# Optimization experiments

Hardware: AMD Instinct MI355X
Metric: run time of the kernel (lower is better)

## Reference

```python
import jax, jax.numpy as jnp
import numpy as np

T, H = 4096, 2048  # seq_len, hidden/feature size (hidden == features per module code)

def setup_inputs() -> dict:
    key = jax.random.key(0)
    k1, k2, k3 = jax.random.split(key, 3)
    s = 1.0 / np.sqrt(H).astype(np.float32)
    return {
        "x": jax.random.normal(k1, (T, H), jnp.float32),
        "c0": jnp.zeros((H,), jnp.float32),
        "h0": jnp.zeros((H,), jnp.float32),
        "Wi": jax.random.normal(k2, (H, 4 * H), jnp.float32) * s,  # input kernel, gates [i,f,g,o]
        "Wh": jax.random.normal(k3, (H, 4 * H), jnp.float32) * s,  # recurrent kernel
        "b": jnp.zeros((4 * H,), jnp.float32),
    }

def reference(x, c0, h0, Wi, Wh, b):
    # Faithful to flax.linen.OptimizedLSTMCell scanned over time (gate order i,f,g,o).
    def step(carry, xt):
        c, h = carry
        y = xt @ Wi + h @ Wh + b          # (4H,)
        i, f, g, o = jnp.split(y, 4)
        i = jax.nn.sigmoid(i)
        f = jax.nn.sigmoid(f)
        g = jnp.tanh(g)
        o = jax.nn.sigmoid(o)
        c_new = f * c + i * g
        h_new = o * jnp.tanh(c_new)
        return (c_new, h_new), h_new

    (c_f, h_f), ys = jax.lax.scan(step, (c0, h0), x)
    return c_f, h_f, ys
```

## Files before the change

### kernel.cpp

```cpp
#include <hip/hip_runtime.h>
#include <math.h>

#define T_STEPS 4096
#define HDIM    2048
#define KDIM    2048
#define NG      8192
#define NREC    2048
#define NSLOT   3

typedef unsigned long long ull;

__global__ void init_ws5(const float* __restrict__ h0,
                         uint2* __restrict__ recs) {
    int d = blockIdx.x * blockDim.x + threadIdx.x;
    if (d < NSLOT * NREC) {
        int slot = d >> 11;
        int r = d & (NREC - 1);
        uint2 v;
        if (slot == 2) {
            v.x = __float_as_uint(h0[r]);
            v.y = 0u;
        } else {
            v.x = 0u;
            v.y = 0xFFFFFFFFu;
        }
        recs[d] = v;
    }
}

__global__ __launch_bounds__(256) void gemm_xwi(
    const float* __restrict__ X, const float* __restrict__ Wi,
    const float* __restrict__ bias, float* __restrict__ Y)
{
    __shared__ float As[16][65];
    __shared__ __align__(16) float Bs[16][64];
    const int tid = threadIdx.x;
    const int m0 = blockIdx.y * 64;
    const int n0 = blockIdx.x * 64;
    const int tx4 = (tid & 15) * 4;
    const int ty4 = (tid >> 4) * 4;
    const int am = tid >> 2, ak = (tid & 3) * 4;
    const int bk = tid >> 4, bn = (tid & 15) * 4;

    float acc[4][4];
#pragma unroll
    for (int i = 0; i < 4; ++i)
#pragma unroll
        for (int j = 0; j < 4; ++j) acc[i][j] = 0.f;

    for (int kt = 0; kt < KDIM; kt += 16) {
        float4 av = *reinterpret_cast<const float4*>(&X[(size_t)(m0 + am) * KDIM + kt + ak]);
        float4 bv = *reinterpret_cast<const float4*>(&Wi[(size_t)(kt + bk) * NG + n0 + bn]);
        __syncthreads();
        As[ak + 0][am] = av.x; As[ak + 1][am] = av.y;
        As[ak + 2][am] = av.z; As[ak + 3][am] = av.w;
        *reinterpret_cast<float4*>(&Bs[bk][bn]) = bv;
        __syncthreads();
#pragma unroll
        for (int k = 0; k < 16; ++k) {
            float a0 = As[k][ty4 + 0], a1 = As[k][ty4 + 1];
            float a2 = As[k][ty4 + 2], a3 = As[k][ty4 + 3];
            float4 b4 = *reinterpret_cast<const float4*>(&Bs[k][tx4]);
            acc[0][0] = fmaf(a0, b4.x, acc[0][0]); acc[0][1] = fmaf(a0, b4.y, acc[0][1]);
            acc[0][2] = fmaf(a0, b4.z, acc[0][2]); acc[0][3] = fmaf(a0, b4.w, acc[0][3]);
            acc[1][0] = fmaf(a1, b4.x, acc[1][0]); acc[1][1] = fmaf(a1, b4.y, acc[1][1]);
            acc[1][2] = fmaf(a1, b4.z, acc[1][2]); acc[1][3] = fmaf(a1, b4.w, acc[1][3]);
            acc[2][0] = fmaf(a2, b4.x, acc[2][0]); acc[2][1] = fmaf(a2, b4.y, acc[2][1]);
            acc[2][2] = fmaf(a2, b4.z, acc[2][2]); acc[2][3] = fmaf(a2, b4.w, acc[2][3]);
            acc[3][0] = fmaf(a3, b4.x, acc[3][0]); acc[3][1] = fmaf(a3, b4.y, acc[3][1]);
            acc[3][2] = fmaf(a3, b4.z, acc[3][2]); acc[3][3] = fmaf(a3, b4.w, acc[3][3]);
        }
    }
    float4 bb = *reinterpret_cast<const float4*>(&bias[n0 + tx4]);
#pragma unroll
    for (int i = 0; i < 4; ++i) {
        float4 o;
        o.x = acc[i][0] + bb.x; o.y = acc[i][1] + bb.y;
        o.z = acc[i][2] + bb.z; o.w = acc[i][3] + bb.w;
        *reinterpret_cast<float4*>(&Y[(size_t)(m0 + ty4 + i) * NG + n0 + tx4]) = o;
    }
}

__device__ __forceinline__ float fsigm(float x) { return 1.f / (1.f + __expf(-x)); }
__device__ __forceinline__ float ftanh(float x) {
    float ax = fabsf(x);
    float e  = __expf(2.f * ax);
    float t  = (e - 1.f) / (e + 1.f);
    t = (ax > 15.f) ? 1.f : t;
    return copysignf(t, x);
}

__global__ __launch_bounds__(512)
__attribute__((amdgpu_waves_per_eu(2, 2)))
void lstm_persistent(
    const float* __restrict__ Y,
    const float* __restrict__ c0,
    const float* __restrict__ Wh,
    uint2* __restrict__ recs,
    float* __restrict__ out)
{
    const int b    = blockIdx.x;
    const int tid  = threadIdx.x;
    const int lane = tid & 63;
    const int w    = tid >> 6;
    const int gg   = w >> 1;
    const int hg   = w & 1;
    const int nbase = (gg << 11) + (b << 3) + (hg << 2);

    __shared__ __align__(16) float hlds[HDIM];
    __shared__ float gates[32];
    __shared__ float c_s[8];
    __shared__ float hlast[8];

    float4 wreg[32];
#pragma unroll
    for (int j = 0; j < 8; ++j)
#pragma unroll
        for (int m = 0; m < 4; ++m) {
            const size_t k = (size_t)(4 * lane + 256 * j + m);
            wreg[j * 4 + m] = *reinterpret_cast<const float4*>(&Wh[k * NG + nbase]);
        }
#pragma unroll
    for (int i = 0; i < 32; ++i) {
        asm volatile("" : "+v"(wreg[i].x), "+v"(wreg[i].y),
                          "+v"(wreg[i].z), "+v"(wreg[i].w));
    }

    if (tid < 8) c_s[tid] = c0[b * 8 + tid];
    __syncthreads();

    int rs = 2;
    int ws = 0;

    for (int t = 0; t < T_STEPS; ++t) {
        float yv = 0.f;
        if (lane < 4) yv = Y[(size_t)t * NG + nbase + lane];

        {
            const uint2* rb = recs + (size_t)rs * NREC;
            const uint2* p0 = rb + 2 * tid;
            const uint2* p1 = rb + 1024 + 2 * tid;
            const unsigned expt = (unsigned)t;
            uint4 ra, rc;
            for (;;) {
                asm volatile("global_load_dwordx4 %0, %2, off sc0 sc1\n\t"
                             "global_load_dwordx4 %1, %3, off sc0 sc1\n\t"
                             "s_waitcnt vmcnt(0)"
                             : "=&v"(ra), "=&v"(rc)
                             : "v"(p0), "v"(p1) : "memory");
                if (__all((ra.y == expt) & (ra.w == expt) &
                          (rc.y == expt) & (rc.w == expt))) break;
                __builtin_amdgcn_s_sleep(1);
            }
            float2 d0; d0.x = __uint_as_float(ra.x); d0.y = __uint_as_float(ra.z);
            float2 d1; d1.x = __uint_as_float(rc.x); d1.y = __uint_as_float(rc.z);
            *reinterpret_cast<float2*>(&hlds[2 * tid])        = d0;
            *reinterpret_cast<float2*>(&hlds[1024 + 2 * tid]) = d1;
        }
        __syncthreads();

        float4 acc; acc.x = acc.y = acc.z = acc.w = 0.f;
#pragma unroll
        for (int j = 0; j < 8; ++j) {
            float4 h4 = reinterpret_cast<const float4*>(hlds)[lane + 64 * j];
            float4 w0 = wreg[4 * j + 0], w1 = wreg[4 * j + 1];
            float4 w2 = wreg[4 * j + 2], w3 = wreg[4 * j + 3];
            acc.x = fmaf(h4.x, w0.x, acc.x); acc.x = fmaf(h4.y, w1.x, acc.x);
            acc.x = fmaf(h4.z, w2.x, acc.x); acc.x = fmaf(h4.w, w3.x, acc.x);
            acc.y = fmaf(h4.x, w0.y, acc.y); acc.y = fmaf(h4.y, w1.y, acc.y);
            acc.y = fmaf(h4.z, w2.y, acc.y); acc.y = fmaf(h4.w, w3.y, acc.y);
            acc.z = fmaf(h4.x, w0.z, acc.z); acc.z = fmaf(h4.y, w1.z, acc.z);
            acc.z = fmaf(h4.z, w2.z, acc.z); acc.z = fmaf(h4.w, w3.z, acc.z);
            acc.w = fmaf(h4.x, w0.w, acc.w); acc.w = fmaf(h4.y, w1.w, acc.w);
            acc.w = fmaf(h4.z, w2.w, acc.w); acc.w = fmaf(h4.w, w3.w, acc.w);
        }
#pragma unroll
        for (int off = 32; off >= 1; off >>= 1) {
            acc.x += __shfl_xor(acc.x, off);
            acc.y += __shfl_xor(acc.y, off);
            acc.z += __shfl_xor(acc.z, off);
            acc.w += __shfl_xor(acc.w, off);
        }
        if (lane < 4) {
            float v = (lane == 0) ? acc.x : (lane == 1) ? acc.y
                    : (lane == 2) ? acc.z : acc.w;
            gates[gg * 8 + hg * 4 + lane] = v + yv;
        }
        __syncthreads();

        if (tid < 8) {
            float iv = gates[0 * 8 + tid];
            float fv = gates[1 * 8 + tid];
            float gv = gates[2 * 8 + tid];
            float ov = gates[3 * 8 + tid];
            float cn = fsigm(fv) * c_s[tid] + fsigm(iv) * ftanh(gv);
            float hn = fsigm(ov) * ftanh(cn);
            c_s[tid] = cn;
            hlast[tid] = hn;
            ull rec = ((ull)(unsigned)(t + 1) << 32) | (ull)__float_as_uint(hn);
            uint2* dst = recs + (size_t)ws * NREC + b * 8 + tid;
            asm volatile("global_store_dwordx2 %0, %1, off sc0 sc1"
                         :: "v"(dst), "v"(rec) : "memory");
            __builtin_nontemporal_store(hn, &out[2 * HDIM + (size_t)t * HDIM + b * 8 + tid]);
        }

        rs = ws;
        ws = (ws == 2) ? 0 : ws + 1;
    }

    if (tid < 8) {
        out[b * 8 + tid]        = c_s[tid];
        out[HDIM + b * 8 + tid] = hlast[tid];
    }
}

extern "C" void kernel_launch(void* const* d_in, const int* in_sizes, int n_in,
                              void* d_out, int out_size, void* d_ws, size_t ws_size,
                              hipStream_t stream) {
    const float* x   = (const float*)d_in[0];
    const float* c0  = (const float*)d_in[1];
    const float* h0  = (const float*)d_in[2];
    const float* Wi  = (const float*)d_in[3];
    const float* Wh  = (const float*)d_in[4];
    const float* bia = (const float*)d_in[5];
    float* out = (float*)d_out;

    char* base = (char*)d_ws;
    float* Y = (float*)base;
    base += (size_t)T_STEPS * NG * sizeof(float);
    uint2* recs = (uint2*)base;

    const int initN = NSLOT * NREC;
    hipLaunchKernelGGL(init_ws5, dim3((initN + 511) / 512), dim3(512), 0, stream,
                       h0, recs);
    hipLaunchKernelGGL(gemm_xwi, dim3(NG / 64, T_STEPS / 64), dim3(256), 0, stream,
                       x, Wi, bia, Y);

    void* args[] = { (void*)&Y, (void*)&c0, (void*)&Wh,
                     (void*)&recs, (void*)&out };
    (void)hipLaunchCooperativeKernel((const void*)lstm_persistent, dim3(256), dim3(512),
                                     args, 0, stream);
}
```

Baseline: 13.92 ms.

## Enlarge GEMM tiles to 128x128 and give each LSTM wave one hidden unit

```diff
diff --git a/kernel.cpp b/kernel.cpp
--- a/kernel.cpp
+++ b/kernel.cpp
@@ -32,52 +32,62 @@
     const float* __restrict__ X, const float* __restrict__ Wi,
     const float* __restrict__ bias, float* __restrict__ Y)
 {
-    __shared__ float As[16][65];
-    __shared__ __align__(16) float Bs[16][64];
+    __shared__ float As[16][132];
+    __shared__ __align__(16) float Bs[16][128];
     const int tid = threadIdx.x;
-    const int m0 = blockIdx.y * 64;
-    const int n0 = blockIdx.x * 64;
-    const int tx4 = (tid & 15) * 4;
-    const int ty4 = (tid >> 4) * 4;
-    const int am = tid >> 2, ak = (tid & 3) * 4;
-    const int bk = tid >> 4, bn = (tid & 15) * 4;
-
-    float acc[4][4];
-#pragma unroll
-    for (int i = 0; i < 4; ++i)
-#pragma unroll
-        for (int j = 0; j < 4; ++j) acc[i][j] = 0.f;
+    const int m0 = blockIdx.y * 128;
+    const int n0 = blockIdx.x * 128;
+    const int tx = tid & 15;
+    const int ty = tid >> 4;
+    const int ar = tid >> 2, ak = (tid & 3) * 4;
+    const int bk = tid >> 5, bn = (tid & 31) * 4;
+
+    float acc[8][8];
+#pragma unroll
+    for (int i = 0; i < 8; ++i)
+#pragma unroll
+        for (int j = 0; j < 8; ++j) acc[i][j] = 0.f;
 
     for (int kt = 0; kt < KDIM; kt += 16) {
-        float4 av = *reinterpret_cast<const float4*>(&X[(size_t)(m0 + am) * KDIM + kt + ak]);
-        float4 bv = *reinterpret_cast<const float4*>(&Wi[(size_t)(kt + bk) * NG + n0 + bn]);
+        float4 a0 = *reinterpret_cast<const float4*>(&X[(size_t)(m0 + ar) * KDIM + kt + ak]);
+        float4 a1 = *reinterpret_cast<const float4*>(&X[(size_t)(m0 + ar + 64) * KDIM + kt + ak]);
+        float4 b0 = *reinterpret_cast<const float4*>(&Wi[(size_t)(kt + bk) * NG + n0 + bn]);
+        float4 b1 = *reinterpret_cast<const float4*>(&Wi[(size_t)(kt + bk + 8) * NG + n0 + bn]);
         __syncthreads();
-        As[ak + 0][am] = av.x; As[ak + 1][am] = av.y;
-        As[ak + 2][am] = av.z; As[ak + 3][am] = av.w;
-        *reinterpret_cast<float4*>(&Bs[bk][bn]) = bv;
+        As[ak + 0][ar] = a0.x; As[ak + 1][ar] = a0.y;
+        As[ak + 2][ar] = a0.z; As[ak + 3][ar] = a0.w;
+        As[ak + 0][ar + 64] = a1.x; As[ak + 1][ar + 64] = a1.y;
+        As[ak + 2][ar + 64] = a1.z; As[ak + 3][ar + 64] = a1.w;
+        *reinterpret_cast<float4*>(&Bs[bk][bn])     = b0;
+        *reinterpret_cast<float4*>(&Bs[bk + 8][bn]) = b1;
         __syncthreads();
 #pragma unroll
         for (int k = 0; k < 16; ++k) {
-            float a0 = As[k][ty4 + 0], a1 = As[k][ty4 + 1];
-            float a2 = As[k][ty4 + 2], a3 = As[k][ty4 + 3];
-            float4 b4 = *reinterpret_cast<const float4*>(&Bs[k][tx4]);
-            acc[0][0] = fmaf(a0, b4.x, acc[0][0]); acc[0][1] = fmaf(a0, b4.y, acc[0][1]);
-            acc[0][2] = fmaf(a0, b4.z, acc[0][2]); acc[0][3] = fmaf(a0, b4.w, acc[0][3]);
-            acc[1][0] = fmaf(a1, b4.x, acc[1][0]); acc[1][1] = fmaf(a1, b4.y, acc[1][1]);
-            acc[1][2] = fmaf(a1, b4.z, acc[1][2]); acc[1][3] = fmaf(a1, b4.w, acc[1][3]);
-            acc[2][0] = fmaf(a2, b4.x, acc[2][0]); acc[2][1] = fmaf(a2, b4.y, acc[2][1]);
-            acc[2][2] = fmaf(a2, b4.z, acc[2][2]); acc[2][3] = fmaf(a2, b4.w, acc[2][3]);
-            acc[3][0] = fmaf(a3, b4.x, acc[3][0]); acc[3][1] = fmaf(a3, b4.y, acc[3][1]);
-            acc[3][2] = fmaf(a3, b4.z, acc[3][2]); acc[3][3] = fmaf(a3, b4.w, acc[3][3]);
-        }
-    }
-    float4 bb = *reinterpret_cast<const float4*>(&bias[n0 + tx4]);
-#pragma unroll
-    for (int i = 0; i < 4; ++i) {
-        float4 o;
-        o.x = acc[i][0] + bb.x; o.y = acc[i][1] + bb.y;
-        o.z = acc[i][2] + bb.z; o.w = acc[i][3] + bb.w;
-        *reinterpret_cast<float4*>(&Y[(size_t)(m0 + ty4 + i) * NG + n0 + tx4]) = o;
+            float4 aA = *reinterpret_cast<const float4*>(&As[k][ty * 8]);
+            float4 aB = *reinterpret_cast<const float4*>(&As[k][ty * 8 + 4]);
+            float4 bA = *reinterpret_cast<const float4*>(&Bs[k][tx * 8]);
+            float4 bB = *reinterpret_cast<const float4*>(&Bs[k][tx * 8 + 4]);
+            float am[8] = { aA.x, aA.y, aA.z, aA.w, aB.x, aB.y, aB.z, aB.w };
+            float bv[8] = { bA.x, bA.y, bA.z, bA.w, bB.x, bB.y, bB.z, bB.w };
+#pragma unroll
+            for (int i = 0; i < 8; ++i)
+#pragma unroll
+                for (int j = 0; j < 8; ++j)
+                    acc[i][j] = fmaf(am[i], bv[j], acc[i][j]);
+        }
+    }
+    float4 bb0 = *reinterpret_cast<const float4*>(&bias[n0 + tx * 8]);
+    float4 bb1 = *reinterpret_cast<const float4*>(&bias[n0 + tx * 8 + 4]);
+#pragma unroll
+    for (int i = 0; i < 8; ++i) {
+        float4 o0, o1;
+        o0.x = acc[i][0] + bb0.x; o0.y = acc[i][1] + bb0.y;
+        o0.z = acc[i][2] + bb0.z; o0.w = acc[i][3] + bb0.w;
+        o1.x = acc[i][4] + bb1.x; o1.y = acc[i][5] + bb1.y;
+        o1.z = acc[i][6] + bb1.z; o1.w = acc[i][7] + bb1.w;
+        float* yr = &Y[(size_t)(m0 + ty * 8 + i) * NG + n0 + tx * 8];
+        *reinterpret_cast<float4*>(yr)     = o0;
+        *reinterpret_cast<float4*>(yr + 4) = o1;
     }
 }
 
@@ -103,30 +113,24 @@
     const int tid  = threadIdx.x;
     const int lane = tid & 63;
     const int w    = tid >> 6;
-    const int gg   = w >> 1;
-    const int hg   = w & 1;
-    const int nbase = (gg << 11) + (b << 3) + (hg << 2);
-
-    __shared__ __align__(16) float hlds[HDIM];
-    __shared__ float gates[32];
-    __shared__ float c_s[8];
-    __shared__ float hlast[8];
-
-    float4 wreg[32];
-#pragma unroll
-    for (int j = 0; j < 8; ++j)
-#pragma unroll
-        for (int m = 0; m < 4; ++m) {
-            const size_t k = (size_t)(4 * lane + 256 * j + m);
-            wreg[j * 4 + m] = *reinterpret_cast<const float4*>(&Wh[k * NG + nbase]);
-        }
-#pragma unroll
-    for (int i = 0; i < 32; ++i) {
-        asm volatile("" : "+v"(wreg[i].x), "+v"(wreg[i].y),
-                          "+v"(wreg[i].z), "+v"(wreg[i].w));
-    }
-
-    if (tid < 8) c_s[tid] = c0[b * 8 + tid];
+    const int e    = b * 8 + w;
+
+    __shared__ __align__(16) float hbuf[2][HDIM];
+
+    float wc[32][4];
+#pragma unroll
+    for (int j = 0; j < 32; ++j) {
+        const float* wp = &Wh[(size_t)(64 * j + lane) * NG + e];
+        wc[j][0] = wp[0];
+        wc[j][1] = wp[2048];
+        wc[j][2] = wp[4096];
+        wc[j][3] = wp[6144];
+        asm volatile("" : "+v"(wc[j][0]), "+v"(wc[j][1]),
+                          "+v"(wc[j][2]), "+v"(wc[j][3]));
+    }
+
+    float c_r = c0[e];
+    float h_r = 0.f;
     __syncthreads();
 
     int rs = 2;
@@ -134,8 +138,9 @@
 
     for (int t = 0; t < T_STEPS; ++t) {
         float yv = 0.f;
-        if (lane < 4) yv = Y[(size_t)t * NG + nbase + lane];
-
+        if (lane < 4) yv = Y[(size_t)t * NG + (lane << 11) + e];
+
+        float* hb = hbuf[t & 1];
         {
             const uint2* rb = recs + (size_t)rs * NREC;
             const uint2* p0 = rb + 2 * tid;
@@ -154,63 +159,53 @@
             }
             float2 d0; d0.x = __uint_as_float(ra.x); d0.y = __uint_as_float(ra.z);
             float2 d1; d1.x = __uint_as_float(rc.x); d1.y = __uint_as_float(rc.z);
-            *reinterpret_cast<float2*>(&hlds[2 * tid])        = d0;
-            *reinterpret_cast<float2*>(&hlds[1024 + 2 * tid]) = d1;
+            *reinterpret_cast<float2*>(&hb[2 * tid])        = d0;
+            *reinterpret_cast<float2*>(&hb[1024 + 2 * tid]) = d1;
         }
         __syncthreads();
 
-        float4 acc; acc.x = acc.y = acc.z = acc.w = 0.f;
-#pragma unroll
-        for (int j = 0; j < 8; ++j) {
-            float4 h4 = reinterpret_cast<const float4*>(hlds)[lane + 64 * j];
-            float4 w0 = wreg[4 * j + 0], w1 = wreg[4 * j + 1];
-            float4 w2 = wreg[4 * j + 2], w3 = wreg[4 * j + 3];
-            acc.x = fmaf(h4.x, w0.x, acc.x); acc.x = fmaf(h4.y, w1.x, acc.x);
-            acc.x = fmaf(h4.z, w2.x, acc.x); acc.x = fmaf(h4.w, w3.x, acc.x);
-            acc.y = fmaf(h4.x, w0.y, acc.y); acc.y = fmaf(h4.y, w1.y, acc.y);
-            acc.y = fmaf(h4.z, w2.y, acc.y); acc.y = fmaf(h4.w, w3.y, acc.y);
-            acc.z = fmaf(h4.x, w0.z, acc.z); acc.z = fmaf(h4.y, w1.z, acc.z);
-            acc.z = fmaf(h4.z, w2.z, acc.z); acc.z = fmaf(h4.w, w3.z, acc.z);
-            acc.w = fmaf(h4.x, w0.w, acc.w); acc.w = fmaf(h4.y, w1.w, acc.w);
-            acc.w = fmaf(h4.z, w2.w, acc.w); acc.w = fmaf(h4.w, w3.w, acc.w);
+        float a0 = 0.f, a1 = 0.f, a2 = 0.f, a3 = 0.f;
+#pragma unroll
+        for (int j = 0; j < 32; ++j) {
+            float hj = hb[64 * j + lane];
+            a0 = fmaf(hj, wc[j][0], a0);
+            a1 = fmaf(hj, wc[j][1], a1);
+            a2 = fmaf(hj, wc[j][2], a2);
+            a3 = fmaf(hj, wc[j][3], a3);
         }
 #pragma unroll
         for (int off = 32; off >= 1; off >>= 1) {
-            acc.x += __shfl_xor(acc.x, off);
-            acc.y += __shfl_xor(acc.y, off);
-            acc.z += __shfl_xor(acc.z, off);
-            acc.w += __shfl_xor(acc.w, off);
-        }
-        if (lane < 4) {
-            float v = (lane == 0) ? acc.x : (lane == 1) ? acc.y
-                    : (lane == 2) ? acc.z : acc.w;
-            gates[gg * 8 + hg * 4 + lane] = v + yv;
-        }
-        __syncthreads();
-
-        if (tid < 8) {
-            float iv = gates[0 * 8 + tid];
-            float fv = gates[1 * 8 + tid];
-            float gv = gates[2 * 8 + tid];
-            float ov = gates[3 * 8 + tid];
-            float cn = fsigm(fv) * c_s[tid] + fsigm(iv) * ftanh(gv);
+            a0 += __shfl_xor(a0, off);
+            a1 += __shfl_xor(a1, off);
+            a2 += __shfl_xor(a2, off);
+            a3 += __shfl_xor(a3, off);
+        }
+        float sg = ((lane == 0) ? a0 : (lane == 1) ? a1
+                  : (lane == 2) ? a2 : a3) + yv;
+        float iv = __shfl(sg, 0);
+        float fv = __shfl(sg, 1);
+        float gv = __shfl(sg, 2);
+        float ov = __shfl(sg, 3);
+
+        if (lane == 0) {
+            float cn = fsigm(fv) * c_r + fsigm(iv) * ftanh(gv);
             float hn = fsigm(ov) * ftanh(cn);
-            c_s[tid] = cn;
-            hlast[tid] = hn;
+            c_r = cn;
+            h_r = hn;
             ull rec = ((ull)(unsigned)(t + 1) << 32) | (ull)__float_as_uint(hn);
-            uint2* dst = recs + (size_t)ws * NREC + b * 8 + tid;
+            uint2* dst = recs + (size_t)ws * NREC + e;
             asm volatile("global_store_dwordx2 %0, %1, off sc0 sc1"
                          :: "v"(dst), "v"(rec) : "memory");
-            __builtin_nontemporal_store(hn, &out[2 * HDIM + (size_t)t * HDIM + b * 8 + tid]);
+            __builtin_nontemporal_store(hn, &out[2 * HDIM + (size_t)t * HDIM + e]);
         }
 
         rs = ws;
         ws = (ws == 2) ? 0 : ws + 1;
     }
 
-    if (tid < 8) {
-        out[b * 8 + tid]        = c_s[tid];
-        out[HDIM + b * 8 + tid] = hlast[tid];
+    if (lane == 0) {
+        out[e]        = c_r;
+        out[HDIM + e] = h_r;
     }
 }
 
@@ -233,7 +228,7 @@
     const int initN = NSLOT * NREC;
     hipLaunchKernelGGL(init_ws5, dim3((initN + 511) / 512), dim3(512), 0, stream,
                        h0, recs);
-    hipLaunchKernelGGL(gemm_xwi, dim3(NG / 64, T_STEPS / 64), dim3(256), 0, stream,
+    hipLaunchKernelGGL(gemm_xwi, dim3(NG / 128, T_STEPS / 128), dim3(256), 0, stream,
                        x, Wi, bia, Y);
 
     void* args[] = { (void*)&Y, (void*)&c0, (void*)&Wh,
```

New measurement: 20.72 ms. +48.9%, slower.
